# Kernel optimization log

Measured on AMD Instinct MI355X. Metric: run time of the kernel, lower is better.

## Reference

```python
import jax, jax.numpy as jnp
import numpy as np

NUM_USER = 1000
NUM_NODES = 3000
NUM_REL = 5
HID = 500
OUT = 75
NUM_BASIS = 2
NUM_EDGES = 200000


def setup_inputs() -> dict:
    key = jax.random.key(0)
    ks = jax.random.split(key, 8)
    x = jnp.arange(NUM_NODES, dtype=jnp.int64 if jax.config.jax_enable_x64 else jnp.int32)
    edge_index = jax.random.randint(ks[0], (2, NUM_EDGES), 0, NUM_NODES)
    edge_type = jax.random.randint(ks[1], (NUM_EDGES,), 0, NUM_REL)
    edge_norm = jax.random.uniform(ks[2], (NUM_EDGES,), dtype=jnp.float32)
    # RGC ordinal basis weights: W_r = cumsum of per-relation bases (GCMC ordinal weight sharing)
    ord_basis = 0.01 * jax.random.normal(ks[3], (NUM_REL, NUM_NODES, HID), dtype=jnp.float32)
    # DenseLayer weight (no bias), shared for user/item branches
    W_dense = 0.05 * jax.random.normal(ks[4], (HID, OUT), dtype=jnp.float32)
    # BiDecoder basis decomposition
    basis_matrix = 0.1 * jax.random.normal(ks[5], (NUM_BASIS, OUT * OUT), dtype=jnp.float32)
    coefs = 0.1 * jax.random.normal(ks[6], (NUM_REL, NUM_BASIS), dtype=jnp.float32)
    return {"x": x, "edge_index": edge_index, "edge_type": edge_type,
            "edge_norm": edge_norm, "ord_basis": ord_basis, "W_dense": W_dense,
            "basis_matrix": basis_matrix, "coefs": coefs}


def reference(x, edge_index, edge_type, edge_norm, ord_basis, W_dense, basis_matrix, coefs):
    R, N, H = ord_basis.shape
    # --- RGCLayer: ordinal cumulative weight sharing ---
    weight = jnp.cumsum(ord_basis, axis=0).reshape(R * N, H)  # (R*N, H)
    src, dst = edge_index[0], edge_index[1]
    idx = edge_type * N + x[src]                      # row lookup = one-hot feature matmul
    msgs = weight[idx] * edge_norm[:, None]           # (E, H) gather, memory-bound
    agg = jax.ops.segment_sum(msgs, dst, num_segments=N)  # scatter-add to target nodes
    feat = jax.nn.relu(agg)                           # (N, H)
    # --- separate users / items, DenseLayer ---
    u = jax.nn.relu(feat[:NUM_USER] @ W_dense)        # (U, OUT)
    i = jax.nn.relu(feat[NUM_USER:] @ W_dense)        # (I, OUT)
    # --- BiDecoder: basis-combination bilinear scores per relation ---
    D = W_dense.shape[1]
    Q = jnp.einsum('rb,bk->rk', coefs, basis_matrix).reshape(R, D, D)
    out = jnp.einsum('ud,rde,ie->uir', u, Q, i)       # (U, I, R)
    return out.reshape(u.shape[0] * i.shape[0], R)
```

## Files before the change

### kernel.cpp

```cpp
#include <hip/hip_runtime.h>
#include <hip/hip_bf16.h>

#define NUSER 1000
#define NNODES 3000
#define NREL 5
#define HID 500
#define DOUT 75
#define NBASIS 2
#define NEDGES 200000
#define NITEM (NNODES - NUSER)
#define NH (NNODES * HID)

__global__ void k_cumsum(const float4* __restrict__ basis, float4* __restrict__ weight) {
    int i = blockIdx.x * blockDim.x + threadIdx.x;
    if (i >= NH / 4) return;
    float4 s = make_float4(0.f, 0.f, 0.f, 0.f);
#pragma unroll
    for (int r = 0; r < NREL; ++r) {
        float4 b = basis[r * (NH / 4) + i];
        s.x += b.x; s.y += b.y; s.z += b.z; s.w += b.w;
        weight[r * (NH / 4) + i] = s;
    }
}

__global__ void k_degree(const int* __restrict__ dst, int* __restrict__ deg) {
    int e = blockIdx.x * blockDim.x + threadIdx.x;
    if (e < NEDGES) atomicAdd(&deg[dst[e]], 1);
}

__global__ void k_scan(const int* __restrict__ deg, int* __restrict__ offs,
                       int* __restrict__ cursor) {
    __shared__ int tmp[1024];
    int t = threadIdx.x;
    int base = t * 3;
    int a = (base     < NNODES) ? deg[base]     : 0;
    int b = (base + 1 < NNODES) ? deg[base + 1] : 0;
    int c = (base + 2 < NNODES) ? deg[base + 2] : 0;
    int s = a + b + c;
    tmp[t] = s;
    __syncthreads();
    for (int d = 1; d < 1024; d <<= 1) {
        int x = (t >= d) ? tmp[t - d] : 0;
        __syncthreads();
        tmp[t] += x;
        __syncthreads();
    }
    int excl = tmp[t] - s;
    if (base < NNODES)     { offs[base]     = excl;         cursor[base]     = excl; }
    if (base + 1 < NNODES) { offs[base + 1] = excl + a;     cursor[base + 1] = excl + a; }
    if (base + 2 < NNODES) { offs[base + 2] = excl + a + b; cursor[base + 2] = excl + a + b; }
    if (t == 1023) offs[NNODES] = tmp[1023];
}

__global__ void k_fill(const int* __restrict__ src, const int* __restrict__ dst,
                       const int* __restrict__ etype, const float* __restrict__ enorm,
                       const int* __restrict__ x,
                       int* __restrict__ cursor, int* __restrict__ csr_row,
                       float* __restrict__ csr_norm) {
    int e = blockIdx.x * blockDim.x + threadIdx.x;
    if (e >= NEDGES) return;
    int d = dst[e];
    int pos = atomicAdd(&cursor[d], 1);
    csr_row[pos] = etype[e] * NNODES + x[src[e]];
    csr_norm[pos] = enorm[e];
}

__global__ __launch_bounds__(256) void k_agg(const float* __restrict__ weight,
                                             const int* __restrict__ offs,
                                             const int* __restrict__ csr_row,
                                             const float* __restrict__ csr_norm,
                                             float* __restrict__ feat) {
    int n = blockIdx.x;
    int t = threadIdx.x;
    int beg = offs[n], end = offs[n + 1];
    int c1 = t + 256;
    float acc0 = 0.f, acc1 = 0.f;
    for (int p = beg; p < end; ++p) {
        int row = csr_row[p];
        float w = csr_norm[p];
        const float* wr = weight + (size_t)row * HID;
        acc0 += wr[t] * w;
        if (c1 < HID) acc1 += wr[c1] * w;
    }
    feat[(size_t)n * HID + t] = fmaxf(acc0, 0.f);
    if (c1 < HID) feat[(size_t)n * HID + c1] = fmaxf(acc1, 0.f);
}

#define DN 4
__global__ __launch_bounds__(128) void k_dense(const float* __restrict__ feat,
                                               const float* __restrict__ W,
                                               float* __restrict__ uv) {
    __shared__ float lds[DN][HID];
    int nb = blockIdx.x * DN;
    int t = threadIdx.x;
    for (int j = t; j < DN * HID; j += 128) {
        int nn = j / HID, d = j % HID;
        lds[nn][d] = (nb + nn < NNODES) ? feat[(size_t)(nb + nn) * HID + d] : 0.f;
    }
    __syncthreads();
    if (t < DOUT) {
        float a0 = 0.f, a1 = 0.f, a2 = 0.f, a3 = 0.f;
        for (int d = 0; d < HID; ++d) {
            float w = W[d * DOUT + t];
            a0 += lds[0][d] * w;
            a1 += lds[1][d] * w;
            a2 += lds[2][d] * w;
            a3 += lds[3][d] * w;
        }
        if (nb + 0 < NNODES) uv[(nb + 0) * DOUT + t] = fmaxf(a0, 0.f);
        if (nb + 1 < NNODES) uv[(nb + 1) * DOUT + t] = fmaxf(a1, 0.f);
        if (nb + 2 < NNODES) uv[(nb + 2) * DOUT + t] = fmaxf(a2, 0.f);
        if (nb + 3 < NNODES) uv[(nb + 3) * DOUT + t] = fmaxf(a3, 0.f);
    }
}

__global__ void k_T(const float* __restrict__ uv, const float* __restrict__ bm,
                    float* __restrict__ T) {
    int i = blockIdx.x * blockDim.x + threadIdx.x;
    if (i >= NBASIS * NUSER * DOUT) return;
    int b = i / (NUSER * DOUT);
    int rem = i % (NUSER * DOUT);
    int u = rem / DOUT;
    int e = rem % DOUT;
    float acc = 0.f;
    for (int d = 0; d < DOUT; ++d)
        acc += uv[u * DOUT + d] * bm[b * DOUT * DOUT + d * DOUT + e];
    T[i] = acc;
}

#define UT 32
#define IT 128
#define EC 25
__global__ __launch_bounds__(256) void k_dec(const float* __restrict__ T,
                                             const float* __restrict__ uv,
                                             const float* __restrict__ coefs,
                                             float* __restrict__ out) {
    __shared__ float As[NBASIS][UT][EC];
    __shared__ float Is[IT][EC];
    int t = threadIdx.x;
    int ti = t & 15, tu = t >> 4;
    int ub = blockIdx.y * UT;
    int ib = blockIdx.x * IT;

    float acc[NBASIS][2][8];
#pragma unroll
    for (int b = 0; b < NBASIS; ++b)
#pragma unroll
        for (int uu = 0; uu < 2; ++uu)
#pragma unroll
            for (int k = 0; k < 8; ++k) acc[b][uu][k] = 0.f;

    for (int e0 = 0; e0 < DOUT; e0 += EC) {
        for (int j = t; j < NBASIS * UT * EC; j += 256) {
            int b = j / (UT * EC);
            int rem = j % (UT * EC);
            int uu = rem / EC, c = rem % EC;
            int u = ub + uu;
            As[b][uu][c] = (u < NUSER) ? T[(b * NUSER + u) * DOUT + e0 + c] : 0.f;
        }
        for (int j = t; j < IT * EC; j += 256) {
            int ii = j / EC, c = j % EC;
            int i = ib + ii;
            Is[ii][c] = (i < NITEM) ? uv[(size_t)(NUSER + i) * DOUT + e0 + c] : 0.f;
        }
        __syncthreads();
        for (int c = 0; c < EC; ++c) {
            float av[NBASIS][2];
#pragma unroll
            for (int b = 0; b < NBASIS; ++b) {
                av[b][0] = As[b][tu][c];
                av[b][1] = As[b][tu + 16][c];
            }
            float iv[8];
#pragma unroll
            for (int k = 0; k < 8; ++k) iv[k] = Is[ti + 16 * k][c];
#pragma unroll
            for (int b = 0; b < NBASIS; ++b)
#pragma unroll
                for (int uu = 0; uu < 2; ++uu)
#pragma unroll
                    for (int k = 0; k < 8; ++k)
                        acc[b][uu][k] += av[b][uu] * iv[k];
        }
        __syncthreads();
    }

    float cf[NREL][NBASIS];
#pragma unroll
    for (int r = 0; r < NREL; ++r)
#pragma unroll
        for (int b = 0; b < NBASIS; ++b) cf[r][b] = coefs[r * NBASIS + b];

#pragma unroll
    for (int uu = 0; uu < 2; ++uu) {
        int u = ub + tu + uu * 16;
        if (u >= NUSER) continue;
#pragma unroll
        for (int k = 0; k < 8; ++k) {
            int i = ib + ti + 16 * k;
            if (i >= NITEM) continue;
            size_t base = ((size_t)u * NITEM + i) * NREL;
            float s0 = acc[0][uu][k], s1 = acc[1][uu][k];
#pragma unroll
            for (int r = 0; r < NREL; ++r)
                out[base + r] = cf[r][0] * s0 + cf[r][1] * s1;
        }
    }
}

extern "C" void kernel_launch(void* const* d_in, const int* in_sizes, int n_in,
                              void* d_out, int out_size, void* d_ws, size_t ws_size,
                              hipStream_t stream) {
    const int*   x     = (const int*)d_in[0];
    const int*   ei    = (const int*)d_in[1];
    const int*   etype = (const int*)d_in[2];
    const float* enorm = (const float*)d_in[3];
    const float* basis = (const float*)d_in[4];
    const float* Wd    = (const float*)d_in[5];
    const float* bm    = (const float*)d_in[6];
    const float* coefs = (const float*)d_in[7];
    float* out = (float*)d_out;

    float* weight   = (float*)d_ws;
    float* feat     = weight + 7500000;
    float* uv       = feat + 1500000;
    float* T        = uv + 225000;
    float* csr_norm = T + 150000;
    int*   csr_row  = (int*)(csr_norm + 200000);
    int*   deg      = csr_row + 200000;
    int*   offs     = deg + 3000;
    int*   cursor   = offs + 3001;

    const int* src = ei;
    const int* dst = ei + NEDGES;

    hipMemsetAsync(deg, 0, NNODES * sizeof(int), stream);
    k_cumsum<<<(NH / 4 + 255) / 256, 256, 0, stream>>>((const float4*)basis, (float4*)weight);
    k_degree<<<(NEDGES + 255) / 256, 256, 0, stream>>>(dst, deg);
    k_scan<<<1, 1024, 0, stream>>>(deg, offs, cursor);
    k_fill<<<(NEDGES + 255) / 256, 256, 0, stream>>>(src, dst, etype, enorm, x, cursor,
                                                     csr_row, csr_norm);
    k_agg<<<NNODES, 256, 0, stream>>>(weight, offs, csr_row, csr_norm, feat);
    k_dense<<<(NNODES + DN - 1) / DN, 128, 0, stream>>>(feat, Wd, uv);
    k_T<<<(NBASIS * NUSER * DOUT + 255) / 256, 256, 0, stream>>>(uv, bm, T);
    k_dec<<<dim3((NITEM + IT - 1) / IT, (NUSER + UT - 1) / UT), 256, 0, stream>>>(T, uv, coefs, out);
}
```

Before: 287.0 us.

## Vectorize aggregation, shuffle-based scan, fold memset, retile dense and decoder

```diff
diff --git a/kernel.cpp b/kernel.cpp
--- a/kernel.cpp
+++ b/kernel.cpp
@@ -11,8 +11,10 @@
 #define NITEM (NNODES - NUSER)
 #define NH (NNODES * HID)
 
-__global__ void k_cumsum(const float4* __restrict__ basis, float4* __restrict__ weight) {
+__global__ void k_cumsum(const float4* __restrict__ basis, float4* __restrict__ weight,
+                         int* __restrict__ deg) {
     int i = blockIdx.x * blockDim.x + threadIdx.x;
+    if (i < NNODES) deg[i] = 0;
     if (i >= NH / 4) return;
     float4 s = make_float4(0.f, 0.f, 0.f, 0.f);
 #pragma unroll
@@ -28,28 +30,42 @@
     if (e < NEDGES) atomicAdd(&deg[dst[e]], 1);
 }
 
-__global__ void k_scan(const int* __restrict__ deg, int* __restrict__ offs,
-                       int* __restrict__ cursor) {
-    __shared__ int tmp[1024];
+__global__ __launch_bounds__(1024) void k_scan(const int* __restrict__ deg,
+                                               int* __restrict__ offs,
+                                               int* __restrict__ cursor) {
+    __shared__ int wsum[16];
     int t = threadIdx.x;
     int base = t * 3;
     int a = (base     < NNODES) ? deg[base]     : 0;
     int b = (base + 1 < NNODES) ? deg[base + 1] : 0;
     int c = (base + 2 < NNODES) ? deg[base + 2] : 0;
     int s = a + b + c;
-    tmp[t] = s;
-    __syncthreads();
-    for (int d = 1; d < 1024; d <<= 1) {
-        int x = (t >= d) ? tmp[t - d] : 0;
-        __syncthreads();
-        tmp[t] += x;
-        __syncthreads();
-    }
-    int excl = tmp[t] - s;
+    int lane = t & 63, wid = t >> 6;
+    int v = s;
+#pragma unroll
+    for (int d = 1; d < 64; d <<= 1) {
+        int x = __shfl_up(v, d);
+        if (lane >= d) v += x;
+    }
+    if (lane == 63) wsum[wid] = v;
+    __syncthreads();
+    if (t < 16) {
+        int w = wsum[t];
+#pragma unroll
+        for (int d = 1; d < 16; d <<= 1) {
+            int x = __shfl_up(w, d);
+            if (t >= d) w += x;
+        }
+        wsum[t] = w;
+    }
+    __syncthreads();
+    int woff = wid ? wsum[wid - 1] : 0;
+    int incl = v + woff;
+    int excl = incl - s;
     if (base < NNODES)     { offs[base]     = excl;         cursor[base]     = excl; }
     if (base + 1 < NNODES) { offs[base + 1] = excl + a;     cursor[base + 1] = excl + a; }
     if (base + 2 < NNODES) { offs[base + 2] = excl + a + b; cursor[base + 2] = excl + a + b; }
-    if (t == 1023) offs[NNODES] = tmp[1023];
+    if (t == 1023) offs[NNODES] = incl;
 }
 
 __global__ void k_fill(const int* __restrict__ src, const int* __restrict__ dst,
@@ -65,52 +81,61 @@
     csr_norm[pos] = enorm[e];
 }
 
-__global__ __launch_bounds__(256) void k_agg(const float* __restrict__ weight,
+__global__ __launch_bounds__(256) void k_agg(const float4* __restrict__ w4,
                                              const int* __restrict__ offs,
                                              const int* __restrict__ csr_row,
                                              const float* __restrict__ csr_norm,
-                                             float* __restrict__ feat) {
+                                             float4* __restrict__ feat4) {
+    __shared__ float4 part[125];
     int n = blockIdx.x;
     int t = threadIdx.x;
     int beg = offs[n], end = offs[n + 1];
-    int c1 = t + 256;
-    float acc0 = 0.f, acc1 = 0.f;
-    for (int p = beg; p < end; ++p) {
-        int row = csr_row[p];
-        float w = csr_norm[p];
-        const float* wr = weight + (size_t)row * HID;
-        acc0 += wr[t] * w;
-        if (c1 < HID) acc1 += wr[c1] * w;
-    }
-    feat[(size_t)n * HID + t] = fmaxf(acc0, 0.f);
-    if (c1 < HID) feat[(size_t)n * HID + c1] = fmaxf(acc1, 0.f);
-}
-
-#define DN 4
-__global__ __launch_bounds__(128) void k_dense(const float* __restrict__ feat,
+    int half = t >> 7;
+    int lane = t & 127;
+    float4 acc = make_float4(0.f, 0.f, 0.f, 0.f);
+    if (lane < 125) {
+        for (int p = beg + half; p < end; p += 2) {
+            int row = csr_row[p];
+            float w = csr_norm[p];
+            float4 v = w4[(size_t)row * 125 + lane];
+            acc.x += v.x * w; acc.y += v.y * w; acc.z += v.z * w; acc.w += v.w * w;
+        }
+    }
+    if (half == 1 && lane < 125) part[lane] = acc;
+    __syncthreads();
+    if (half == 0 && lane < 125) {
+        float4 o = part[lane];
+        acc.x = fmaxf(acc.x + o.x, 0.f);
+        acc.y = fmaxf(acc.y + o.y, 0.f);
+        acc.z = fmaxf(acc.z + o.z, 0.f);
+        acc.w = fmaxf(acc.w + o.w, 0.f);
+        feat4[(size_t)n * 125 + lane] = acc;
+    }
+}
+
+#define DN 8
+__global__ __launch_bounds__(256) void k_dense(const float* __restrict__ feat,
                                                const float* __restrict__ W,
                                                float* __restrict__ uv) {
     __shared__ float lds[DN][HID];
     int nb = blockIdx.x * DN;
     int t = threadIdx.x;
-    for (int j = t; j < DN * HID; j += 128) {
-        int nn = j / HID, d = j % HID;
-        lds[nn][d] = (nb + nn < NNODES) ? feat[(size_t)(nb + nn) * HID + d] : 0.f;
-    }
-    __syncthreads();
-    if (t < DOUT) {
-        float a0 = 0.f, a1 = 0.f, a2 = 0.f, a3 = 0.f;
+    const float4* f4 = (const float4*)(feat + (size_t)nb * HID);
+    float4* l4 = (float4*)&lds[0][0];
+    for (int j = t; j < DN * HID / 4; j += 256) l4[j] = f4[j];
+    __syncthreads();
+    if (t < 225) {
+        int g = t / 75, o = t % 75;
+        float a0 = 0.f, a1 = 0.f, a2 = 0.f;
         for (int d = 0; d < HID; ++d) {
-            float w = W[d * DOUT + t];
-            a0 += lds[0][d] * w;
-            a1 += lds[1][d] * w;
-            a2 += lds[2][d] * w;
-            a3 += lds[3][d] * w;
-        }
-        if (nb + 0 < NNODES) uv[(nb + 0) * DOUT + t] = fmaxf(a0, 0.f);
-        if (nb + 1 < NNODES) uv[(nb + 1) * DOUT + t] = fmaxf(a1, 0.f);
-        if (nb + 2 < NNODES) uv[(nb + 2) * DOUT + t] = fmaxf(a2, 0.f);
-        if (nb + 3 < NNODES) uv[(nb + 3) * DOUT + t] = fmaxf(a3, 0.f);
+            float w = W[d * DOUT + o];
+            a0 += lds[g][d] * w;
+            a1 += lds[g + 3][d] * w;
+            a2 += lds[(g + 6) & 7][d] * w;
+        }
+        uv[(nb + g) * DOUT + o]     = fmaxf(a0, 0.f);
+        uv[(nb + g + 3) * DOUT + o] = fmaxf(a1, 0.f);
+        if (g < 2) uv[(nb + g + 6) * DOUT + o] = fmaxf(a2, 0.f);
     }
 }
 
@@ -138,17 +163,12 @@
     __shared__ float As[NBASIS][UT][EC];
     __shared__ float Is[IT][EC];
     int t = threadIdx.x;
-    int ti = t & 15, tu = t >> 4;
+    int ti = t & 31;
+    int tu = t >> 5;
     int ub = blockIdx.y * UT;
     int ib = blockIdx.x * IT;
 
-    float acc[NBASIS][2][8];
-#pragma unroll
-    for (int b = 0; b < NBASIS; ++b)
-#pragma unroll
-        for (int uu = 0; uu < 2; ++uu)
-#pragma unroll
-            for (int k = 0; k < 8; ++k) acc[b][uu][k] = 0.f;
+    float acc[NBASIS][4][4] = {};
 
     for (int e0 = 0; e0 < DOUT; e0 += EC) {
         for (int j = t; j < NBASIS * UT * EC; j += 256) {
@@ -165,21 +185,21 @@
         }
         __syncthreads();
         for (int c = 0; c < EC; ++c) {
-            float av[NBASIS][2];
-#pragma unroll
-            for (int b = 0; b < NBASIS; ++b) {
-                av[b][0] = As[b][tu][c];
-                av[b][1] = As[b][tu + 16][c];
-            }
-            float iv[8];
-#pragma unroll
-            for (int k = 0; k < 8; ++k) iv[k] = Is[ti + 16 * k][c];
+            float av[NBASIS][4];
 #pragma unroll
             for (int b = 0; b < NBASIS; ++b)
 #pragma unroll
-                for (int uu = 0; uu < 2; ++uu)
-#pragma unroll
-                    for (int k = 0; k < 8; ++k)
+                for (int uu = 0; uu < 4; ++uu)
+                    av[b][uu] = As[b][tu * 4 + uu][c];
+            float iv[4];
+#pragma unroll
+            for (int k = 0; k < 4; ++k) iv[k] = Is[ti + 32 * k][c];
+#pragma unroll
+            for (int b = 0; b < NBASIS; ++b)
+#pragma unroll
+                for (int uu = 0; uu < 4; ++uu)
+#pragma unroll
+                    for (int k = 0; k < 4; ++k)
                         acc[b][uu][k] += av[b][uu] * iv[k];
         }
         __syncthreads();
@@ -192,12 +212,12 @@
         for (int b = 0; b < NBASIS; ++b) cf[r][b] = coefs[r * NBASIS + b];
 
 #pragma unroll
-    for (int uu = 0; uu < 2; ++uu) {
-        int u = ub + tu + uu * 16;
+    for (int uu = 0; uu < 4; ++uu) {
+        int u = ub + tu * 4 + uu;
         if (u >= NUSER) continue;
 #pragma unroll
-        for (int k = 0; k < 8; ++k) {
-            int i = ib + ti + 16 * k;
+        for (int k = 0; k < 4; ++k) {
+            int i = ib + ti + 32 * k;
             if (i >= NITEM) continue;
             size_t base = ((size_t)u * NITEM + i) * NREL;
             float s0 = acc[0][uu][k], s1 = acc[1][uu][k];
@@ -234,14 +254,15 @@
     const int* src = ei;
     const int* dst = ei + NEDGES;
 
-    hipMemsetAsync(deg, 0, NNODES * sizeof(int), stream);
-    k_cumsum<<<(NH / 4 + 255) / 256, 256, 0, stream>>>((const float4*)basis, (float4*)weight);
+    k_cumsum<<<(NH / 4 + 255) / 256, 256, 0, stream>>>((const float4*)basis,
+                                                       (float4*)weight, deg);
     k_degree<<<(NEDGES + 255) / 256, 256, 0, stream>>>(dst, deg);
     k_scan<<<1, 1024, 0, stream>>>(deg, offs, cursor);
     k_fill<<<(NEDGES + 255) / 256, 256, 0, stream>>>(src, dst, etype, enorm, x, cursor,
                                                      csr_row, csr_norm);
-    k_agg<<<NNODES, 256, 0, stream>>>(weight, offs, csr_row, csr_norm, feat);
-    k_dense<<<(NNODES + DN - 1) / DN, 128, 0, stream>>>(feat, Wd, uv);
+    k_agg<<<NNODES, 256, 0, stream>>>((const float4*)weight, offs, csr_row, csr_norm,
+                                      (float4*)feat);
+    k_dense<<<NNODES / DN, 256, 0, stream>>>(feat, Wd, uv);
     k_T<<<(NBASIS * NUSER * DOUT + 255) / 256, 256, 0, stream>>>(uv, bm, T);
     k_dec<<<dim3((NITEM + IT - 1) / IT, (NUSER + UT - 1) / UT), 256, 0, stream>>>(T, uv, coefs, out);
 }
```

New measurement: 273.4 us. 4.7% less time.
